# Kernel tuning notes

Hardware: AMD Instinct MI355X
Metric: run time of the kernel (lower is better)

The kernel has to match this reference:

```python
import jax, jax.numpy as jnp
import numpy as np

B, L, D = 1, 2048, 2048
NH, NKV, HD = 32, 8, 64          # heads, kv heads, head_dim = D // NH
THETA = 50000.0
EPS = 1e-5
SCALE = HD ** -0.5


def _rope(x):
    # traditional (interleaved-pair) RoPE; x: (B, H, L, HD)
    hd = x.shape[-1]
    pos = jnp.arange(x.shape[2], dtype=jnp.float32)
    inv = THETA ** (-jnp.arange(0, hd, 2, dtype=jnp.float32) / hd)
    ang = pos[:, None] * inv[None, :]              # (L, HD/2)
    cos, sin = jnp.cos(ang), jnp.sin(ang)
    x1, x2 = x[..., ::2], x[..., 1::2]
    r1 = x1 * cos - x2 * sin
    r2 = x1 * sin + x2 * cos
    return jnp.stack([r1, r2], axis=-1).reshape(x.shape)


def _rmsnorm(x, w):
    return x * jax.lax.rsqrt(jnp.mean(x * x, axis=-1, keepdims=True) + EPS) * w


def setup_inputs() -> dict:
    key = jax.random.key(0)
    ks = jax.random.split(key, 5)
    x = jax.random.normal(ks[0], (B, L, D), dtype=jnp.float32)
    w_qkv = jax.random.normal(ks[1], (NH * HD + 2 * NKV * HD, D), dtype=jnp.float32) * 0.02
    w_out = jax.random.normal(ks[2], (D, D), dtype=jnp.float32) * 0.02
    q_gamma = 1.0 + 0.02 * jax.random.normal(ks[3], (HD,), dtype=jnp.float32)
    k_gamma = 1.0 + 0.02 * jax.random.normal(ks[4], (HD,), dtype=jnp.float32)
    mask = jnp.tril(jnp.ones((L, L), dtype=bool))   # causal
    return {"x": x, "w_qkv": w_qkv, "w_out": w_out,
            "q_gamma": q_gamma, "k_gamma": k_gamma, "mask": mask}


def reference(x, w_qkv, w_out, q_gamma, k_gamma, mask):
    b, l, d = x.shape
    qkv = x @ w_qkv.T                               # fused QKV proj (no bias)
    q, k, v = jnp.split(qkv, [NH * HD, NH * HD + NKV * HD], axis=-1)
    q = q.reshape(b, l, NH, HD).transpose(0, 2, 1, 3)     # (B,NH,L,HD)
    k = k.reshape(b, l, NKV, HD).transpose(0, 2, 1, 3)    # (B,NKV,L,HD)
    v = v.reshape(b, l, NKV, HD).transpose(0, 2, 1, 3)
    q = _rmsnorm(_rope(q), q_gamma)
    k = _rmsnorm(_rope(k), k_gamma)
    g = NH // NKV                                   # GQA group size
    qg = q.reshape(b, NKV, g, l, HD)
    scores = jnp.einsum('bkgqd,bkld->bkgql', qg, k) * SCALE
    scores = jnp.where(mask, scores, -jnp.inf)
    attn = jax.nn.softmax(scores, axis=-1)
    out = jnp.einsum('bkgql,bkld->bkgqd', attn, v)  # (B,NKV,g,L,HD)
    out = out.reshape(b, NH, l, HD).transpose(0, 2, 1, 3).reshape(b, l, d)
    return out @ w_out.T
```

## Files before the change

### kernel.cpp

```cpp
#include <hip/hip_runtime.h>

using bf16   = __bf16;
using bf16x4 = __bf16 __attribute__((ext_vector_type(4)));
using bf16x8 = __bf16 __attribute__((ext_vector_type(8)));
using f32x4  = float __attribute__((ext_vector_type(4)));
using f32x16 = float __attribute__((ext_vector_type(16)));
using u32x2  = unsigned int __attribute__((ext_vector_type(2)));
using u32x4  = unsigned int __attribute__((ext_vector_type(4)));

#define L_SEQ  2048
#define DMODEL 2048
#define NQH    32
#define NKVH   8
#define HDIM   64
#define QKV_N  3072

#define KVF_HSTRIDE (64 * 4 * 64 * 8)

__device__ __forceinline__ void gload_lds16(const void* g, void* lds) {
  __builtin_amdgcn_global_load_lds((__attribute__((address_space(1))) void*)(g),
                                   (__attribute__((address_space(3))) void*)(lds),
                                   16, 0, 0);
}

__device__ __forceinline__ unsigned pack2(float a, float b) {
  union { bf16 h[2]; unsigned u; } x;
  x.h[0] = (bf16)a; x.h[1] = (bf16)b;
  return x.u;
}

__global__ void cvt_f32_bf16(const float* __restrict__ in, bf16* __restrict__ out, long n) {
  const long stride = (long)gridDim.x * blockDim.x;
  const long n4 = n >> 2;
  for (long i = (long)blockIdx.x * blockDim.x + threadIdx.x; i < n4; i += stride) {
    const float4 v = reinterpret_cast<const float4*>(in)[i];
    bf16x4 o = { (bf16)v.x, (bf16)v.y, (bf16)v.z, (bf16)v.w };
    reinterpret_cast<bf16x4*>(out)[i] = o;
  }
}

template <typename OutT>
__global__ __launch_bounds__(256)
void gemm_bt(const bf16* __restrict__ A, const bf16* __restrict__ B,
             OutT* __restrict__ C, int M, int N, int K) {
  __shared__ bf16 As[2][128 * 64];
  __shared__ bf16 Bs[2][64 * 64];
  const int tid = threadIdx.x;
  const int w = tid >> 6, l = tid & 63;
  const int wr = w >> 1, wc = w & 1;
  const int lq = l & 15, lg = l >> 4;
  const long m0 = (long)blockIdx.y * 128;
  const long n0 = (long)blockIdx.x * 64;

  const int lrow = l >> 3;
  const int scol = ((l & 7) ^ lrow) << 3;

  f32x4 acc[4][2];
#pragma unroll
  for (int i = 0; i < 4; ++i)
#pragma unroll
    for (int j = 0; j < 2; ++j) acc[i][j] = f32x4{0.f, 0.f, 0.f, 0.f};

#pragma unroll
  for (int i = 0; i < 4; ++i) {
    const int r0 = (w * 4 + i) * 8;
    gload_lds16(A + (m0 + r0 + lrow) * (long)K + scol, &As[0][r0 * 64]);
  }
#pragma unroll
  for (int i = 0; i < 2; ++i) {
    const int r0 = (w * 2 + i) * 8;
    gload_lds16(B + (n0 + r0 + lrow) * (long)K + scol, &Bs[0][r0 * 64]);
  }
  __syncthreads();

  const int nk = K >> 6;
  for (int t = 0; t < nk; ++t) {
    const int cur = t & 1, nxt = cur ^ 1;
    const int k1 = (t + 1 < nk) ? (t + 1) * 64 : t * 64;
#pragma unroll
    for (int i = 0; i < 4; ++i) {
      const int r0 = (w * 4 + i) * 8;
      gload_lds16(A + (m0 + r0 + lrow) * (long)K + k1 + scol, &As[nxt][r0 * 64]);
    }
#pragma unroll
    for (int i = 0; i < 2; ++i) {
      const int r0 = (w * 2 + i) * 8;
      gload_lds16(B + (n0 + r0 + lrow) * (long)K + k1 + scol, &Bs[nxt][r0 * 64]);
    }
#pragma unroll
    for (int kk = 0; kk < 2; ++kk) {
      bf16x8 af[4], bfr[2];
#pragma unroll
      for (int tt = 0; tt < 4; ++tt) {
        const int rowA = wr * 64 + tt * 16 + lq;
        const int blkA = (kk * 4 + lg) ^ (rowA & 7);
        af[tt] = *reinterpret_cast<const bf16x8*>(&As[cur][rowA * 64 + blkA * 8]);
      }
#pragma unroll
      for (int tt = 0; tt < 2; ++tt) {
        const int rowB = wc * 32 + tt * 16 + lq;
        const int blkB = (kk * 4 + lg) ^ (rowB & 7);
        bfr[tt] = *reinterpret_cast<const bf16x8*>(&Bs[cur][rowB * 64 + blkB * 8]);
      }
#pragma unroll
      for (int mt = 0; mt < 4; ++mt)
#pragma unroll
        for (int nt = 0; nt < 2; ++nt)
          acc[mt][nt] = __builtin_amdgcn_mfma_f32_16x16x32_bf16(af[mt], bfr[nt], acc[mt][nt], 0, 0, 0);
    }
    __syncthreads();
  }

#pragma unroll
  for (int mt = 0; mt < 4; ++mt)
#pragma unroll
    for (int r = 0; r < 4; ++r) {
      const long row = m0 + wr * 64 + mt * 16 + lg * 4 + r;
#pragma unroll
      for (int nt = 0; nt < 2; ++nt) {
        const long col = n0 + wc * 32 + nt * 16 + lq;
        C[row * (long)N + col] = (OutT)acc[mt][nt][r];
      }
    }
}

__global__ __launch_bounds__(256)
void rope_rms(const bf16* __restrict__ qkv, const float* __restrict__ qg,
              const float* __restrict__ kg, bf16* __restrict__ qo, bf16* __restrict__ kfr) {
  const int gid = blockIdx.x * 4 + (threadIdx.x >> 6);
  const int lane = threadIdx.x & 63;
  const int pos = gid / 40;
  const int hh = gid % 40;
  const bool isq = hh < 32;
  const int col = isq ? hh * HDIM : NQH * HDIM + (hh - 32) * HDIM;

  float x = (float)qkv[(long)pos * QKV_N + col + lane];
  float p = __shfl_xor(x, 1);
  const float fi = (float)(lane & ~1) * (1.0f / 64.0f);
  const float inv = powf(50000.0f, -fi);
  const float ang = (float)pos * inv;
  const float sn = sinf(ang), cs = cosf(ang);
  const float r = (lane & 1) ? (p * sn + x * cs) : (x * cs - p * sn);

  float ss = r * r;
#pragma unroll
  for (int off = 1; off < 64; off <<= 1) ss += __shfl_xor(ss, off);
  const float scl = rsqrtf(ss * (1.0f / 64.0f) + 1e-5f);
  const float g = isq ? qg[lane] : kg[lane];
  const float o = r * scl * g;

  if (isq) {
    qo[(long)pos * DMODEL + hh * HDIM + lane] = (bf16)(o * 0.18033688011112042f);
  } else {
    const int kvh = hh - 32;
    const int d = lane;
    const int lp = (pos & 31) + (((d >> 3) & 1) << 5);
    const long idx = ((((long)kvh * 64 + (pos >> 5)) * 4 + (d >> 4)) * 64 + lp) * 8 + (d & 7);
    kfr[idx] = (bf16)o;
  }
}

__global__ __launch_bounds__(256)
void repack_v(const bf16* __restrict__ qkv, bf16* __restrict__ vfr) {
  __shared__ bf16 t[32][72];
  const int kvh = blockIdx.x >> 6;
  const int kb = blockIdx.x & 63;
  const int tid = threadIdx.x;

  {
    const int row = tid >> 3;
    const int cc = (tid & 7) * 8;
    const bf16* g = qkv + (long)(kb * 32 + row) * QKV_N + (NQH * HDIM + NKVH * HDIM) + kvh * HDIM + cc;
    *reinterpret_cast<u32x4*>(&t[row][cc]) = *reinterpret_cast<const u32x4*>(g);
  }
  __syncthreads();

  const int f = tid >> 6, l = tid & 63;
  const int s = f >> 1, dh = f & 1;
  const int hi = l >> 5, l31 = l & 31;
  union { bf16 b[8]; u32x4 u; } o;
#pragma unroll
  for (int e = 0; e < 8; ++e) o.b[e] = t[s * 16 + hi * 8 + e][dh * 32 + l31];
  bf16* od = vfr + (((long)(kvh * 64 + kb) * 4 + f) * 64 + l) * 8;
  *reinterpret_cast<u32x4*>(od) = o.u;
}

__global__ __launch_bounds__(256)
void flash_attn(const bf16* __restrict__ Q, const bf16* __restrict__ Kfr,
                const bf16* __restrict__ Vfr, bf16* __restrict__ Og) {
  const int w = threadIdx.x >> 6, l = threadIdx.x & 63;
  const int lane31 = l & 31, hi = l >> 5;
  const int wg = blockIdx.x * 4 + w;
  const int h = wg & 31;
  const int qi = 63 - (wg >> 5);
  const int kvh = h >> 2;
  const int q0 = qi * 32;
  const int q_abs = q0 + lane31;
  const int l8 = l * 8;

  const bf16* qrow = Q + (long)q_abs * DMODEL + h * HDIM + hi * 8;
  bf16x8 qf[4];
#pragma unroll
  for (int c = 0; c < 4; ++c) qf[c] = *reinterpret_cast<const bf16x8*>(qrow + c * 16);

  f32x16 o0, o1;
#pragma unroll
  for (int r = 0; r < 16; ++r) { o0[r] = 0.f; o1[r] = 0.f; }
  float m = -3.0e38f, lsum = 0.f;

  const bf16* kfrh = Kfr + (long)kvh * KVF_HSTRIDE;
  const bf16* vfrh = Vfr + (long)kvh * KVF_HSTRIDE;

  const int nst = qi + 1;

  bf16x8 kc0, kc1, kc2, kc3;
  {
    const bf16* kp = kfrh + l8;
    kc0 = *reinterpret_cast<const bf16x8*>(kp);
    kc1 = *reinterpret_cast<const bf16x8*>(kp + 512);
    kc2 = *reinterpret_cast<const bf16x8*>(kp + 1024);
    kc3 = *reinterpret_cast<const bf16x8*>(kp + 1536);
  }

  for (int sti = 0; sti < nst; ++sti) {
    const int kb0 = sti * 32;

    const bf16* vp = vfrh + (long)sti * 2048 + l8;
    const bf16x8 va0 = *reinterpret_cast<const bf16x8*>(vp);
    const bf16x8 vb0 = *reinterpret_cast<const bf16x8*>(vp + 512);
    const bf16x8 va1 = *reinterpret_cast<const bf16x8*>(vp + 1024);
    const bf16x8 vb1 = *reinterpret_cast<const bf16x8*>(vp + 1536);

    const long knoff = (sti + 1 < nst) ? (long)(sti + 1) * 2048 : 0;
    const bf16* kp = kfrh + knoff + l8;
    const bf16x8 kn0 = *reinterpret_cast<const bf16x8*>(kp);
    const bf16x8 kn1 = *reinterpret_cast<const bf16x8*>(kp + 512);
    const bf16x8 kn2 = *reinterpret_cast<const bf16x8*>(kp + 1024);
    const bf16x8 kn3 = *reinterpret_cast<const bf16x8*>(kp + 1536);

    f32x16 st;
#pragma unroll
    for (int r = 0; r < 16; ++r) st[r] = 0.f;
    st = __builtin_amdgcn_mfma_f32_32x32x16_bf16(kc0, qf[0], st, 0, 0, 0);
    st = __builtin_amdgcn_mfma_f32_32x32x16_bf16(kc1, qf[1], st, 0, 0, 0);
    st = __builtin_amdgcn_mfma_f32_32x32x16_bf16(kc2, qf[2], st, 0, 0, 0);
    st = __builtin_amdgcn_mfma_f32_32x32x16_bf16(kc3, qf[3], st, 0, 0, 0);

    if (kb0 + 31 > q0) {
#pragma unroll
      for (int r = 0; r < 16; ++r) {
        const int k_abs = kb0 + (r & 3) + 8 * (r >> 2) + 4 * hi;
        if (k_abs > q_abs) st[r] = -3.0e38f;
      }
    }

    float mx = st[0];
#pragma unroll
    for (int r = 1; r < 16; ++r) mx = fmaxf(mx, st[r]);
    mx = fmaxf(mx, __shfl_xor(mx, 32));
    if (!__all(mx - m <= 8.0f)) {
      const float mn = fmaxf(m, mx);
      const float al = __builtin_amdgcn_exp2f(m - mn);
      m = mn; lsum *= al;
#pragma unroll
      for (int r = 0; r < 16; ++r) { o0[r] *= al; o1[r] *= al; }
    }
    float p[16];
    float rs = 0.f;
#pragma unroll
    for (int r = 0; r < 16; ++r) { p[r] = __builtin_amdgcn_exp2f(st[r] - m); rs += p[r]; }
    rs += __shfl_xor(rs, 32);
    lsum += rs;

#pragma unroll
    for (int s = 0; s < 2; ++s) {
      const int j = s * 8;
      const unsigned W0 = pack2(p[j + 0], p[j + 1]);
      const unsigned W1 = pack2(p[j + 2], p[j + 3]);
      const unsigned W2 = pack2(p[j + 4], p[j + 5]);
      const unsigned W3 = pack2(p[j + 6], p[j + 7]);
      u32x4 pw;
#if __has_builtin(__builtin_amdgcn_permlane32_swap)
      {
        using i32x2 = int __attribute__((ext_vector_type(2)));
        const i32x2 r02 = __builtin_amdgcn_permlane32_swap((int)W0, (int)W2, false, false);
        const i32x2 r13 = __builtin_amdgcn_permlane32_swap((int)W1, (int)W3, false, false);
        pw = u32x4{ (unsigned)r02[0], (unsigned)r13[0], (unsigned)r02[1], (unsigned)r13[1] };
      }
#else
      {
        const unsigned X0 = (unsigned)__shfl_xor((int)W0, 32);
        const unsigned X1 = (unsigned)__shfl_xor((int)W1, 32);
        const unsigned X2 = (unsigned)__shfl_xor((int)W2, 32);
        const unsigned X3 = (unsigned)__shfl_xor((int)W3, 32);
        pw = u32x4{ hi ? X2 : W0, hi ? X3 : W1, hi ? W2 : X0, hi ? W3 : X1 };
      }
#endif
      const bf16x8 pf = __builtin_bit_cast(bf16x8, pw);
      if (s == 0) {
        o0 = __builtin_amdgcn_mfma_f32_32x32x16_bf16(va0, pf, o0, 0, 0, 0);
        o1 = __builtin_amdgcn_mfma_f32_32x32x16_bf16(vb0, pf, o1, 0, 0, 0);
      } else {
        o0 = __builtin_amdgcn_mfma_f32_32x32x16_bf16(va1, pf, o0, 0, 0, 0);
        o1 = __builtin_amdgcn_mfma_f32_32x32x16_bf16(vb1, pf, o1, 0, 0, 0);
      }
    }

    kc0 = kn0; kc1 = kn1; kc2 = kn2; kc3 = kn3;
  }

  const float rl = 1.0f / lsum;
  bf16* orow = Og + (long)q_abs * DMODEL + h * HDIM;
#pragma unroll
  for (int g = 0; g < 4; ++g) {
    const int d0 = 8 * g + 4 * hi;
    u32x2 s0 = { pack2(o0[4 * g + 0] * rl, o0[4 * g + 1] * rl),
                 pack2(o0[4 * g + 2] * rl, o0[4 * g + 3] * rl) };
    u32x2 s1 = { pack2(o1[4 * g + 0] * rl, o1[4 * g + 1] * rl),
                 pack2(o1[4 * g + 2] * rl, o1[4 * g + 3] * rl) };
    *reinterpret_cast<u32x2*>(orow + d0) = s0;
    *reinterpret_cast<u32x2*>(orow + 32 + d0) = s1;
  }
}

extern "C" void kernel_launch(void* const* d_in, const int* in_sizes, int n_in,
                              void* d_out, int out_size, void* d_ws, size_t ws_size,
                              hipStream_t stream) {
  const float* x       = (const float*)d_in[0];
  const float* w_qkv   = (const float*)d_in[1];
  const float* w_out   = (const float*)d_in[2];
  const float* q_gamma = (const float*)d_in[3];
  const float* k_gamma = (const float*)d_in[4];

  char* ws = (char*)d_ws;
  bf16* xb  = (bf16*)(ws);
  bf16* wqb = (bf16*)(ws + (8ul  << 20));
  bf16* wob = (bf16*)(ws + (20ul << 20));
  bf16* qkv = (bf16*)(ws + (28ul << 20));
  bf16* qb  = (bf16*)(ws + (40ul << 20));
  bf16* kfr = (bf16*)(ws + (48ul << 20));
  bf16* vfr = (bf16*)(ws + (50ul << 20));
  bf16* ao  = (bf16*)(ws + (52ul << 20));
  float* out = (float*)d_out;

  cvt_f32_bf16<<<2048, 256, 0, stream>>>(x, xb, (long)L_SEQ * DMODEL);
  cvt_f32_bf16<<<2048, 256, 0, stream>>>(w_qkv, wqb, (long)QKV_N * DMODEL);
  cvt_f32_bf16<<<2048, 256, 0, stream>>>(w_out, wob, (long)DMODEL * DMODEL);

  gemm_bt<bf16><<<dim3(QKV_N / 64, L_SEQ / 128), 256, 0, stream>>>(xb, wqb, qkv, L_SEQ, QKV_N, DMODEL);

  rope_rms<<<(L_SEQ * 40) / 4, 256, 0, stream>>>(qkv, q_gamma, k_gamma, qb, kfr);
  repack_v<<<NKVH * (L_SEQ / 32), 256, 0, stream>>>(qkv, vfr);

  flash_attn<<<(NQH * (L_SEQ / 32)) / 4, 256, 0, stream>>>(qb, kfr, vfr, ao);

  gemm_bt<float><<<dim3(DMODEL / 64, L_SEQ / 128), 256, 0, stream>>>(ao, wob, out, L_SEQ, DMODEL, DMODEL);
}
```

Baseline: 177.9 us.

## Use two-wave single-buffered GEMM tiles and raise MFMA priority in attention

The GEMM kernel goes from four waves to two, so each wave now computes a 64x64 sub-tile with 16 accumulators. The LDS double buffer is dropped in favour of a single buffer loaded at the top of each k-step behind a barrier. The attention kernel wraps its MFMA groups in s_setprio(1)/s_setprio(0) to favour matrix issue over other waves. Removing the prefetch exposes global-load latency in every k-iteration, which the higher per-wave reuse and lower LDS footprint (more resident blocks) are meant to offset.

```diff
diff --git a/kernel.cpp b/kernel.cpp
--- a/kernel.cpp
+++ b/kernel.cpp
@@ -40,14 +40,13 @@
 }
 
 template <typename OutT>
-__global__ __launch_bounds__(256)
+__global__ __launch_bounds__(128)
 void gemm_bt(const bf16* __restrict__ A, const bf16* __restrict__ B,
              OutT* __restrict__ C, int M, int N, int K) {
-  __shared__ bf16 As[2][128 * 64];
-  __shared__ bf16 Bs[2][64 * 64];
+  __shared__ bf16 As[128 * 64];
+  __shared__ bf16 Bs[64 * 64];
   const int tid = threadIdx.x;
   const int w = tid >> 6, l = tid & 63;
-  const int wr = w >> 1, wc = w & 1;
   const int lq = l & 15, lg = l >> 4;
   const long m0 = (long)blockIdx.y * 128;
   const long n0 = (long)blockIdx.x * 64;
@@ -55,57 +54,40 @@
   const int lrow = l >> 3;
   const int scol = ((l & 7) ^ lrow) << 3;
 
-  f32x4 acc[4][2];
+  f32x4 acc[4][4];
 #pragma unroll
   for (int i = 0; i < 4; ++i)
 #pragma unroll
-    for (int j = 0; j < 2; ++j) acc[i][j] = f32x4{0.f, 0.f, 0.f, 0.f};
-
-#pragma unroll
-  for (int i = 0; i < 4; ++i) {
-    const int r0 = (w * 4 + i) * 8;
-    gload_lds16(A + (m0 + r0 + lrow) * (long)K + scol, &As[0][r0 * 64]);
-  }
-#pragma unroll
-  for (int i = 0; i < 2; ++i) {
-    const int r0 = (w * 2 + i) * 8;
-    gload_lds16(B + (n0 + r0 + lrow) * (long)K + scol, &Bs[0][r0 * 64]);
-  }
-  __syncthreads();
-
-  const int nk = K >> 6;
-  for (int t = 0; t < nk; ++t) {
-    const int cur = t & 1, nxt = cur ^ 1;
-    const int k1 = (t + 1 < nk) ? (t + 1) * 64 : t * 64;
+    for (int j = 0; j < 4; ++j) acc[i][j] = f32x4{0.f, 0.f, 0.f, 0.f};
+
+  for (int k0 = 0; k0 < K; k0 += 64) {
+#pragma unroll
+    for (int i = 0; i < 8; ++i) {
+      const int r0 = (i * 2 + w) * 8;
+      gload_lds16(A + (m0 + r0 + lrow) * (long)K + k0 + scol, &As[r0 * 64]);
+    }
 #pragma unroll
     for (int i = 0; i < 4; ++i) {
-      const int r0 = (w * 4 + i) * 8;
-      gload_lds16(A + (m0 + r0 + lrow) * (long)K + k1 + scol, &As[nxt][r0 * 64]);
-    }
-#pragma unroll
-    for (int i = 0; i < 2; ++i) {
-      const int r0 = (w * 2 + i) * 8;
-      gload_lds16(B + (n0 + r0 + lrow) * (long)K + k1 + scol, &Bs[nxt][r0 * 64]);
-    }
+      const int r0 = (i * 2 + w) * 8;
+      gload_lds16(B + (n0 + r0 + lrow) * (long)K + k0 + scol, &Bs[r0 * 64]);
+    }
+    __syncthreads();
 #pragma unroll
     for (int kk = 0; kk < 2; ++kk) {
-      bf16x8 af[4], bfr[2];
-#pragma unroll
-      for (int tt = 0; tt < 4; ++tt) {
-        const int rowA = wr * 64 + tt * 16 + lq;
+      bf16x8 af[4], bfr[4];
+#pragma unroll
+      for (int t = 0; t < 4; ++t) {
+        const int rowA = w * 64 + t * 16 + lq;
         const int blkA = (kk * 4 + lg) ^ (rowA & 7);
-        af[tt] = *reinterpret_cast<const bf16x8*>(&As[cur][rowA * 64 + blkA * 8]);
-      }
-#pragma unroll
-      for (int tt = 0; tt < 2; ++tt) {
-        const int rowB = wc * 32 + tt * 16 + lq;
+        af[t] = *reinterpret_cast<const bf16x8*>(&As[rowA * 64 + blkA * 8]);
+        const int rowB = t * 16 + lq;
         const int blkB = (kk * 4 + lg) ^ (rowB & 7);
-        bfr[tt] = *reinterpret_cast<const bf16x8*>(&Bs[cur][rowB * 64 + blkB * 8]);
+        bfr[t] = *reinterpret_cast<const bf16x8*>(&Bs[rowB * 64 + blkB * 8]);
       }
 #pragma unroll
       for (int mt = 0; mt < 4; ++mt)
 #pragma unroll
-        for (int nt = 0; nt < 2; ++nt)
+        for (int nt = 0; nt < 4; ++nt)
           acc[mt][nt] = __builtin_amdgcn_mfma_f32_16x16x32_bf16(af[mt], bfr[nt], acc[mt][nt], 0, 0, 0);
     }
     __syncthreads();
@@ -115,10 +97,10 @@
   for (int mt = 0; mt < 4; ++mt)
 #pragma unroll
     for (int r = 0; r < 4; ++r) {
-      const long row = m0 + wr * 64 + mt * 16 + lg * 4 + r;
-#pragma unroll
-      for (int nt = 0; nt < 2; ++nt) {
-        const long col = n0 + wc * 32 + nt * 16 + lq;
+      const long row = m0 + w * 64 + mt * 16 + lg * 4 + r;
+#pragma unroll
+      for (int nt = 0; nt < 4; ++nt) {
+        const long col = n0 + nt * 16 + lq;
         C[row * (long)N + col] = (OutT)acc[mt][nt][r];
       }
     }
@@ -241,10 +223,12 @@
     f32x16 st;
 #pragma unroll
     for (int r = 0; r < 16; ++r) st[r] = 0.f;
+    __builtin_amdgcn_s_setprio(1);
     st = __builtin_amdgcn_mfma_f32_32x32x16_bf16(kc0, qf[0], st, 0, 0, 0);
     st = __builtin_amdgcn_mfma_f32_32x32x16_bf16(kc1, qf[1], st, 0, 0, 0);
     st = __builtin_amdgcn_mfma_f32_32x32x16_bf16(kc2, qf[2], st, 0, 0, 0);
     st = __builtin_amdgcn_mfma_f32_32x32x16_bf16(kc3, qf[3], st, 0, 0, 0);
+    __builtin_amdgcn_s_setprio(0);
 
     if (kb0 + 31 > q0) {
 #pragma unroll
@@ -297,6 +281,7 @@
       }
 #endif
       const bf16x8 pf = __builtin_bit_cast(bf16x8, pw);
+      __builtin_amdgcn_s_setprio(1);
       if (s == 0) {
         o0 = __builtin_amdgcn_mfma_f32_32x32x16_bf16(va0, pf, o0, 0, 0, 0);
         o1 = __builtin_amdgcn_mfma_f32_32x32x16_bf16(vb0, pf, o1, 0, 0, 0);
@@ -304,6 +289,7 @@
         o0 = __builtin_amdgcn_mfma_f32_32x32x16_bf16(va1, pf, o0, 0, 0, 0);
         o1 = __builtin_amdgcn_mfma_f32_32x32x16_bf16(vb1, pf, o1, 0, 0, 0);
       }
+      __builtin_amdgcn_s_setprio(0);
     }
 
     kc0 = kn0; kc1 = kn1; kc2 = kn2; kc3 = kn3;
@@ -347,12 +333,12 @@
   cvt_f32_bf16<<<2048, 256, 0, stream>>>(w_qkv, wqb, (long)QKV_N * DMODEL);
   cvt_f32_bf16<<<2048, 256, 0, stream>>>(w_out, wob, (long)DMODEL * DMODEL);
 
-  gemm_bt<bf16><<<dim3(QKV_N / 64, L_SEQ / 128), 256, 0, stream>>>(xb, wqb, qkv, L_SEQ, QKV_N, DMODEL);
+  gemm_bt<bf16><<<dim3(QKV_N / 64, L_SEQ / 128), 128, 0, stream>>>(xb, wqb, qkv, L_SEQ, QKV_N, DMODEL);
 
   rope_rms<<<(L_SEQ * 40) / 4, 256, 0, stream>>>(qkv, q_gamma, k_gamma, qb, kfr);
   repack_v<<<NKVH * (L_SEQ / 32), 256, 0, stream>>>(qkv, vfr);
 
   flash_attn<<<(NQH * (L_SEQ / 32)) / 4, 256, 0, stream>>>(qb, kfr, vfr, ao);
 
-  gemm_bt<float><<<dim3(DMODEL / 64, L_SEQ / 128), 256, 0, stream>>>(ao, wob, out, L_SEQ, DMODEL, DMODEL);
-}
+  gemm_bt<float><<<dim3(DMODEL / 64, L_SEQ / 128), 128, 0, stream>>>(ao, wob, out, L_SEQ, DMODEL, DMODEL);
+}
```

Result: faster. 171.7 us (-3.5%).
